# Kernel tuning notes

Measured on AMD Instinct MI355X. Metric: run time of the kernel, lower is better.

Reference implementation:

```python
import jax, jax.numpy as jnp
import numpy as np

B, H, W, C = 64, 28, 28, 384
G = 7
N = G * G                  # tokens per window = 49
NH, HD = 12, 32            # heads, head_dim
SCALE = HD ** -0.5
EPS = 1e-5


def _make_bias_coords():
    # biases: all relative (dh, dw) offsets, shape [(2G-1)^2, 2]
    r = np.arange(1 - G, G)
    biases = np.stack(np.meshgrid(r, r, indexing='ij')).reshape(2, -1).T.astype(np.float32)
    # relative_position_index: [N, N] lookup into the bias table
    coords = np.stack(np.meshgrid(np.arange(G), np.arange(G), indexing='ij')).reshape(2, -1)
    rel = coords[:, :, None] - coords[:, None, :]          # [2, N, N]
    rel = rel.transpose(1, 2, 0)                            # [N, N, 2]
    rel[:, :, 0] += G - 1
    rel[:, :, 1] += G - 1
    rel[:, :, 0] *= 2 * G - 1
    idx = rel.sum(-1)                                       # [N, N]
    return jnp.asarray(biases), jnp.asarray(idx, dtype=jnp.int32)

BIASES, REL_IDX = _make_bias_coords()


def _ln(x, g, b):
    m = jnp.mean(x, -1, keepdims=True)
    v = jnp.var(x, -1, keepdims=True)
    return (x - m) * jax.lax.rsqrt(v + EPS) * g + b


def _pos_bias(ppw, ppb, l1g, l1b, p1w, p1b, l2g, l2b, p2w, p2b, l3g, l3b, p3w, p3b):
    # DynamicPosBias with residual=False: pos3(pos2(pos1(pos_proj(biases))))
    pos = BIASES @ ppw + ppb                                # [169, 24]
    pos = jax.nn.relu(_ln(pos, l1g, l1b)) @ p1w + p1b
    pos = jax.nn.relu(_ln(pos, l2g, l2b)) @ p2w + p2b
    pos = jax.nn.relu(_ln(pos, l3g, l3b)) @ p3w + p3b       # [169, NH]
    # gather -> [N, N, NH] -> [NH, N, N]
    return pos[REL_IDX.reshape(-1)].reshape(N, N, NH).transpose(2, 0, 1)


def _forward(x, norm1_g, norm1_b, qkv_w, qkv_b, proj_w, proj_b,
             norm2_g, norm2_b, fc1_w, fc1_b, fc2_w, fc2_b,
             pp_w, pp_b, l1_g, l1_b, p1_w, p1_b, l2_g, l2_b, p2_w, p2_b,
             l3_g, l3_b, p3_w, p3_b):
    shortcut = x
    h = _ln(x, norm1_g, norm1_b).reshape(B, H, W, C)
    # SDA (lsda_flag=0) window partition: [B, H/G, G, W/G, G, C] -> windows
    h = h.reshape(B, H // G, G, W // G, G, C).transpose(0, 1, 3, 2, 4, 5)
    h = h.reshape(-1, N, C)                                 # [B*nW, N, C]
    Bw = h.shape[0]

    qkv = (h @ qkv_w + qkv_b).reshape(Bw, N, 3, NH, HD).transpose(2, 0, 3, 1, 4)
    q, k, v = qkv[0] * SCALE, qkv[1], qkv[2]                # [Bw, NH, N, HD]

    bias = _pos_bias(pp_w, pp_b, l1_g, l1_b, p1_w, p1_b,
                     l2_g, l2_b, p2_w, p2_b, l3_g, l3_b, p3_w, p3_b)
    attn = jnp.einsum('bhnd,bhmd->bhnm', q, k) + bias[None]  # [Bw, NH, N, N]
    attn = jax.nn.softmax(attn, axis=-1)

    o = jnp.einsum('bhnm,bhmd->bhnd', attn, v)
    o = o.transpose(0, 2, 1, 3).reshape(Bw, N, C)
    o = o @ proj_w + proj_b

    # reverse window partition
    o = o.reshape(B, H // G, W // G, G, G, C).transpose(0, 1, 3, 2, 4, 5)
    o = o.reshape(B, H * W, C)

    x = shortcut + o
    y = _ln(x, norm2_g, norm2_b)
    y = jax.nn.gelu(y @ fc1_w + fc1_b, approximate=False) @ fc2_w + fc2_b
    return x + y


def setup_inputs() -> dict:
    key = jax.random.key(0)
    ks = iter(jax.random.split(key, 32))
    s = 0.02
    PD = 24  # pos_dim = (dim // 4) // 4
    MH = 4 * C

    def rn(k, shape):
        return jax.random.normal(k, shape, dtype=jnp.float32) * s

    return {
        'x': jax.random.normal(next(ks), (B, H * W, C), dtype=jnp.float32),
        'norm1_g': jnp.ones((C,), jnp.float32), 'norm1_b': jnp.zeros((C,), jnp.float32),
        'qkv_w': rn(next(ks), (C, 3 * C)), 'qkv_b': jnp.zeros((3 * C,), jnp.float32),
        'proj_w': rn(next(ks), (C, C)), 'proj_b': jnp.zeros((C,), jnp.float32),
        'norm2_g': jnp.ones((C,), jnp.float32), 'norm2_b': jnp.zeros((C,), jnp.float32),
        'fc1_w': rn(next(ks), (C, MH)), 'fc1_b': jnp.zeros((MH,), jnp.float32),
        'fc2_w': rn(next(ks), (MH, C)), 'fc2_b': jnp.zeros((C,), jnp.float32),
        'pp_w': rn(next(ks), (2, PD)), 'pp_b': jnp.zeros((PD,), jnp.float32),
        'l1_g': jnp.ones((PD,), jnp.float32), 'l1_b': jnp.zeros((PD,), jnp.float32),
        'p1_w': rn(next(ks), (PD, PD)), 'p1_b': jnp.zeros((PD,), jnp.float32),
        'l2_g': jnp.ones((PD,), jnp.float32), 'l2_b': jnp.zeros((PD,), jnp.float32),
        'p2_w': rn(next(ks), (PD, PD)), 'p2_b': jnp.zeros((PD,), jnp.float32),
        'l3_g': jnp.ones((PD,), jnp.float32), 'l3_b': jnp.zeros((PD,), jnp.float32),
        'p3_w': rn(next(ks), (PD, NH)), 'p3_b': jnp.zeros((NH,), jnp.float32),
    }


def reference(x, norm1_g, norm1_b, qkv_w, qkv_b, proj_w, proj_b,
              norm2_g, norm2_b, fc1_w, fc1_b, fc2_w, fc2_b,
              pp_w, pp_b, l1_g, l1_b, p1_w, p1_b, l2_g, l2_b, p2_w, p2_b,
              l3_g, l3_b, p3_w, p3_b):
    return _forward(x, norm1_g, norm1_b, qkv_w, qkv_b, proj_w, proj_b,
                    norm2_g, norm2_b, fc1_w, fc1_b, fc2_w, fc2_b,
                    pp_w, pp_b, l1_g, l1_b, p1_w, p1_b, l2_g, l2_b, p2_w, p2_b,
                    l3_g, l3_b, p3_w, p3_b)
```

## Files before the change

kernel.cpp:

```cpp
#include <hip/hip_runtime.h>

typedef unsigned short u16;
typedef short s16x8 __attribute__((ext_vector_type(8)));
typedef short s16x4 __attribute__((ext_vector_type(4)));
typedef float f32x4 __attribute__((ext_vector_type(4)));
typedef float f32x2 __attribute__((ext_vector_type(2)));

#define B_ 64
#define Hh 28
#define Ww 28
#define Cc 384
#define Gg 7
#define Nn 49
#define NH 12
#define HD 32
#define TT 50176
#define NWIN 1024
#define QKV_ELEMS 19267584u
#define SCALE_Q 0.17677669529663687f

__device__ __forceinline__ float b2f(u16 u) {
  union { unsigned int i; float f; } v; v.i = ((unsigned int)u) << 16; return v.f;
}
__device__ __forceinline__ u16 f2b(float f) {
  union { float f; unsigned int i; } v; v.f = f;
  unsigned int r = v.i + 0x7fffu + ((v.i >> 16) & 1u);
  return (u16)(r >> 16);
}

__global__ void transpose_f2b(const float* __restrict__ in, u16* __restrict__ out,
                              int K, int N) {
  int i = blockIdx.x * 256 + threadIdx.x;
  if (i < K * N) {
    int k = i / N, n = i % N;
    out[(size_t)n * K + k] = f2b(in[i]);
  }
}

__global__ __launch_bounds__(256)
void pos_mlp_kernel(const float* __restrict__ pp_w, const float* __restrict__ pp_b,
                    const float* __restrict__ l1g, const float* __restrict__ l1b,
                    const float* __restrict__ p1w, const float* __restrict__ p1b,
                    const float* __restrict__ l2g, const float* __restrict__ l2b,
                    const float* __restrict__ p2w, const float* __restrict__ p2b,
                    const float* __restrict__ l3g, const float* __restrict__ l3b,
                    const float* __restrict__ p3w, const float* __restrict__ p3b,
                    float* __restrict__ pos169) {
  __shared__ float w0[48], bb0[24], g1[24], e1[24], w1[576], bb1[24],
                   g2[24], e2[24], w2[576], bb2[24], g3[24], e3[24], w3[288], bb3[12];
  int tid = threadIdx.x;
  for (int i = tid; i < 48; i += 256) w0[i] = pp_w[i];
  for (int i = tid; i < 24; i += 256) {
    bb0[i] = pp_b[i]; g1[i] = l1g[i]; e1[i] = l1b[i]; bb1[i] = p1b[i];
    g2[i] = l2g[i]; e2[i] = l2b[i]; bb2[i] = p2b[i];
    g3[i] = l3g[i]; e3[i] = l3b[i];
  }
  for (int i = tid; i < 576; i += 256) { w1[i] = p1w[i]; w2[i] = p2w[i]; }
  for (int i = tid; i < 288; i += 256) w3[i] = p3w[i];
  for (int i = tid; i < 12; i += 256) bb3[i] = p3b[i];
  __syncthreads();
  if (tid < 169) {
    float bi = (float)(tid / 13) - 6.f, bj = (float)(tid % 13) - 6.f;
    float cur[24], t[24];
    #pragma unroll
    for (int c = 0; c < 24; c++) cur[c] = bi * w0[c] + bj * w0[24 + c] + bb0[c];

    auto lnrelu = [&](const float* gg, const float* ee) {
      float s = 0.f, sq = 0.f;
      #pragma unroll
      for (int c = 0; c < 24; c++) { s += cur[c]; sq += cur[c] * cur[c]; }
      float mean = s * (1.f / 24.f);
      float var = sq * (1.f / 24.f) - mean * mean;
      float rstd = rsqrtf(var + 1e-5f);
      #pragma unroll
      for (int c = 0; c < 24; c++)
        t[c] = fmaxf(0.f, (cur[c] - mean) * rstd * gg[c] + ee[c]);
    };

    lnrelu(g1, e1);
    #pragma unroll
    for (int o = 0; o < 24; o++) {
      float a = bb1[o];
      #pragma unroll
      for (int c = 0; c < 24; c++) a += t[c] * w1[c * 24 + o];
      cur[o] = a;
    }
    lnrelu(g2, e2);
    #pragma unroll
    for (int o = 0; o < 24; o++) {
      float a = bb2[o];
      #pragma unroll
      for (int c = 0; c < 24; c++) a += t[c] * w2[c * 24 + o];
      cur[o] = a;
    }
    lnrelu(g3, e3);
    #pragma unroll
    for (int h = 0; h < 12; h++) {
      float a = bb3[h];
      #pragma unroll
      for (int c = 0; c < 24; c++) a += t[c] * w3[c * 12 + h];
      pos169[tid * 12 + h] = a;
    }
  }
}

__global__ __launch_bounds__(256)
void ln_kernel(const float* __restrict__ x, const float* __restrict__ g,
               const float* __restrict__ be, u16* __restrict__ out) {
  int wid = threadIdx.x >> 6, lane = threadIdx.x & 63;
  size_t row = (size_t)blockIdx.x * 4 + wid;
  const float* xr = x + row * Cc;
  float v[6];
  float s = 0.f, sq = 0.f;
  #pragma unroll
  for (int p = 0; p < 3; p++) {
    f32x2 u = *(const f32x2*)&xr[p * 128 + lane * 2];
    v[2 * p] = u.x; v[2 * p + 1] = u.y;
    s += u.x + u.y; sq += u.x * u.x + u.y * u.y;
  }
  #pragma unroll
  for (int off = 32; off > 0; off >>= 1) { s += __shfl_xor(s, off); sq += __shfl_xor(sq, off); }
  float mean = s * (1.f / 384.f);
  float var = sq * (1.f / 384.f) - mean * mean;
  float rstd = rsqrtf(var + 1e-5f);
  u16* orow = out + row * Cc;
  #pragma unroll
  for (int p = 0; p < 3; p++) {
    int c = p * 128 + lane * 2;
    f32x2 ug = *(const f32x2*)&g[c];
    f32x2 ub = *(const f32x2*)&be[c];
    float o0 = (v[2 * p] - mean) * rstd * ug.x + ub.x;
    float o1 = (v[2 * p + 1] - mean) * rstd * ug.y + ub.y;
    unsigned int uo = (unsigned int)f2b(o0) | ((unsigned int)f2b(o1) << 16);
    *(unsigned int*)&orow[c] = uo;
  }
}

template <int EPI>
__global__ __launch_bounds__(256, 2)
void gemm_k(const u16* __restrict__ A, const u16* __restrict__ Bt,
            const float* __restrict__ bias, const void* resv, void* outv,
            int M, int N, int K, int rowoff) {
  __shared__ u16 As[128 * 40];
  __shared__ u16 Bs[128 * 40];
  const int tid = threadIdx.x;
  const int mBase = blockIdx.y * 128;
  const int nBase = blockIdx.x * 128;
  const int wid = tid >> 6, lane = tid & 63;
  const int wr = (wid >> 1) * 64, wc = (wid & 1) * 64;
  const int lm = lane & 15, lq = lane >> 4;

  f32x4 acc[4][4] = {};
  for (int k0 = 0; k0 < K; k0 += 32) {
    #pragma unroll
    for (int ss = 0; ss < 2; ss++) {
      int li = tid + ss * 256;
      int r = li >> 2, c8 = (li & 3) * 8;
      *(s16x8*)&As[r * 40 + c8] = *(const s16x8*)&A[(size_t)(mBase + r) * K + k0 + c8];
      *(s16x8*)&Bs[r * 40 + c8] = *(const s16x8*)&Bt[(size_t)(nBase + r) * K + k0 + c8];
    }
    __syncthreads();
    s16x8 af[4], bfr[4];
    #pragma unroll
    for (int i = 0; i < 4; i++) af[i] = *(const s16x8*)&As[(wr + i * 16 + lm) * 40 + lq * 8];
    #pragma unroll
    for (int j = 0; j < 4; j++) bfr[j] = *(const s16x8*)&Bs[(wc + j * 16 + lm) * 40 + lq * 8];
    #pragma unroll
    for (int i = 0; i < 4; i++)
      #pragma unroll
      for (int j = 0; j < 4; j++)
        acc[i][j] = __builtin_amdgcn_mfma_f32_16x16x32_bf16(af[i], bfr[j], acc[i][j], 0, 0, 0);
    __syncthreads();
  }

  int colA[4]; float bvv[4];
  #pragma unroll
  for (int j = 0; j < 4; j++) {
    colA[j] = nBase + wc + j * 16 + lm;
    bvv[j] = bias[colA[j]];
  }

  if constexpr (EPI == 0) {
    u16* out = (u16*)outv;
    size_t offj[4]; float scl[4];
    #pragma unroll
    for (int j = 0; j < 4; j++) {
      int col = colA[j];
      int qi = col / 384, c2 = col % 384;
      int head = c2 >> 5, d = c2 & 31;
      offj[j] = (size_t)qi * QKV_ELEMS + (size_t)head * 1568 + d;
      scl[j] = (qi == 0) ? SCALE_Q : 1.0f;
    }
    #pragma unroll
    for (int i = 0; i < 4; i++) {
      #pragma unroll
      for (int rg = 0; rg < 4; rg++) {
        int t = mBase + wr + i * 16 + lq * 4 + rg;
        int b_ = t / 784, rr = t % 784;
        int hh = rr / 28, ww = rr % 28;
        int widx = b_ * 16 + (hh / 7) * 4 + (ww / 7);
        int n = (hh % 7) * 7 + (ww % 7);
        size_t offr = (size_t)widx * 18816 + n * 32;
        #pragma unroll
        for (int j = 0; j < 4; j++)
          out[offj[j] + offr] = f2b((acc[i][j][rg] + bvv[j]) * scl[j]);
      }
    }
  } else if constexpr (EPI == 1) {
    float* out = (float*)outv;
    const float* res = (const float*)resv;
    #pragma unroll
    for (int i = 0; i < 4; i++) {
      #pragma unroll
      for (int rg = 0; rg < 4; rg++) {
        size_t rb = (size_t)(rowoff + mBase + wr + i * 16 + lq * 4 + rg) * 384;
        #pragma unroll
        for (int j = 0; j < 4; j++) {
          size_t o = rb + colA[j];
          out[o] = acc[i][j][rg] + bvv[j] + res[o];
        }
      }
    }
  } else {
    u16* out = (u16*)outv;
    #pragma unroll
    for (int i = 0; i < 4; i++) {
      #pragma unroll
      for (int rg = 0; rg < 4; rg++) {
        size_t rb = (size_t)(mBase + wr + i * 16 + lq * 4 + rg) * 1536;
        #pragma unroll
        for (int j = 0; j < 4; j++) {
          float v = acc[i][j][rg] + bvv[j];
          float gl = 0.5f * v * (1.0f + erff(v * 0.70710678118654752f));
          out[rb + colA[j]] = f2b(gl);
        }
      }
    }
  }
}

__global__ __launch_bounds__(256, 3)
void attn_mfma(const u16* __restrict__ qkv, const float* __restrict__ pos169,
               u16* __restrict__ attn_out) {
  __shared__ u16 P_l[4][64 * 68];
  __shared__ float bias_l[4][170];
  const int wid = threadIdx.x >> 6, lane = threadIdx.x & 63;
  const int lm = lane & 15, lq = lane >> 4;
  const int pair = blockIdx.x * 4 + wid;
  const int widx = pair / 12, head = pair % 12;
  const u16* qp = qkv + (size_t)widx * 18816 + head * 1568;
  const u16* kp = qp + QKV_ELEMS;
  const u16* vp = kp + QKV_ELEMS;

  for (int i = lane; i < 169; i += 64) bias_l[wid][i] = pos169[i * 12 + head];

  s16x8 aq[4], bk[4];
  #pragma unroll
  for (int i = 0; i < 4; i++) aq[i] = *(const s16x8*)&qp[(i * 16 + lm) * 32 + lq * 8];
  #pragma unroll
  for (int j = 0; j < 4; j++) bk[j] = *(const s16x8*)&kp[(j * 16 + lm) * 32 + lq * 8];

  f32x4 acc[4][4] = {};
  #pragma unroll
  for (int i = 0; i < 4; i++)
    #pragma unroll
    for (int j = 0; j < 4; j++)
      acc[i][j] = __builtin_amdgcn_mfma_f32_16x16x32_bf16(aq[i], bk[j], acc[i][j], 0, 0, 0);

  int mj[4], mhj[4], mwj[4];
  #pragma unroll
  for (int j = 0; j < 4; j++) {
    mj[j] = j * 16 + lm; mhj[j] = mj[j] / 7; mwj[j] = mj[j] - mhj[j] * 7;
  }

  #pragma unroll
  for (int i = 0; i < 4; i++) {
    #pragma unroll
    for (int rg = 0; rg < 4; rg++) {
      int n = i * 16 + lq * 4 + rg;
      int nh = n / 7, nw = n - nh * 7;
      float s[4];
      #pragma unroll
      for (int j = 0; j < 4; j++) {
        int idx = (nh - mhj[j] + 6) * 13 + (nw - mwj[j] + 6);
        idx = min(max(idx, 0), 168);
        s[j] = acc[i][j][rg] + bias_l[wid][idx];
        if (mj[j] >= 49) s[j] = -3.0e30f;
      }
      float mx = fmaxf(fmaxf(s[0], s[1]), fmaxf(s[2], s[3]));
      #pragma unroll
      for (int off = 1; off < 16; off <<= 1) mx = fmaxf(mx, __shfl_xor(mx, off));
      float e[4];
      float sm = 0.f;
      #pragma unroll
      for (int j = 0; j < 4; j++) { e[j] = __expf(s[j] - mx); sm += e[j]; }
      #pragma unroll
      for (int off = 1; off < 16; off <<= 1) sm += __shfl_xor(sm, off);
      float r = 1.0f / sm;
      #pragma unroll
      for (int j = 0; j < 4; j++)
        P_l[wid][n * 68 + mj[j]] = f2b(e[j] * r);
    }
  }

  s16x8 ap[4][2];
  #pragma unroll
  for (int i = 0; i < 4; i++)
    #pragma unroll
    for (int ks = 0; ks < 2; ks++) {
      const u16* p = &P_l[wid][(i * 16 + lm) * 68 + ks * 32 + lq * 8];
      s16x4 lo = *(const s16x4*)p;
      s16x4 hi = *(const s16x4*)(p + 4);
      ap[i][ks] = __builtin_shufflevector(lo, hi, 0, 1, 2, 3, 4, 5, 6, 7);
    }
  s16x8 bv[2][2];
  #pragma unroll
  for (int jt = 0; jt < 2; jt++)
    #pragma unroll
    for (int ks = 0; ks < 2; ks++) {
      s16x8 v;
      #pragma unroll
      for (int jj = 0; jj < 8; jj++)
        v[jj] = (short)vp[(ks * 32 + lq * 8 + jj) * 32 + jt * 16 + lm];
      bv[jt][ks] = v;
    }

  f32x4 o[4][2] = {};
  #pragma unroll
  for (int i = 0; i < 4; i++)
    #pragma unroll
    for (int jt = 0; jt < 2; jt++)
      #pragma unroll
      for (int ks = 0; ks < 2; ks++)
        o[i][jt] = __builtin_amdgcn_mfma_f32_16x16x32_bf16(ap[i][ks], bv[jt][ks], o[i][jt], 0, 0, 0);

  const int b_ = widx >> 4, wq = widx & 15;
  const int hbase = (wq >> 2) * 7, wbase = (wq & 3) * 7;
  #pragma unroll
  for (int i = 0; i < 4; i++) {
    #pragma unroll
    for (int rg = 0; rg < 4; rg++) {
      int n = i * 16 + lq * 4 + rg;
      if (n < 49) {
        int nh = n / 7, nw = n - nh * 7;
        int t = b_ * 784 + (hbase + nh) * 28 + (wbase + nw);
        size_t ob = (size_t)t * 384 + head * 32 + lm;
        attn_out[ob] = f2b(o[i][0][rg]);
        attn_out[ob + 16] = f2b(o[i][1][rg]);
      }
    }
  }
}

extern "C" void kernel_launch(void* const* d_in, const int* in_sizes, int n_in,
                              void* d_out, int out_size, void* d_ws, size_t ws_size,
                              hipStream_t stream) {
  const float* x      = (const float*)d_in[0];
  const float* n1g    = (const float*)d_in[1];
  const float* n1b    = (const float*)d_in[2];
  const float* qkv_w  = (const float*)d_in[3];
  const float* qkv_b  = (const float*)d_in[4];
  const float* proj_w = (const float*)d_in[5];
  const float* proj_b = (const float*)d_in[6];
  const float* n2g    = (const float*)d_in[7];
  const float* n2b    = (const float*)d_in[8];
  const float* fc1_w  = (const float*)d_in[9];
  const float* fc1_b  = (const float*)d_in[10];
  const float* fc2_w  = (const float*)d_in[11];
  const float* fc2_b  = (const float*)d_in[12];

  const size_t SZ_A = 115605504;
  const size_t SZ_B = 38535168;
  char* wsb = (char*)d_ws;
  u16* regA     = (u16*)wsb;
  u16* regB     = (u16*)(wsb + SZ_A);
  float* pos169 = (float*)(wsb + SZ_A + SZ_B);
  u16* qkvT     = (u16*)(wsb + SZ_A + SZ_B + 8192);
  u16* projT    = qkvT + 442368;
  u16* fc1T     = projT + 147456;
  u16* fc2T     = fc1T + 589824;

  float* out = (float*)d_out;

  transpose_f2b<<<1728, 256, 0, stream>>>(qkv_w, qkvT, 384, 1152);
  transpose_f2b<<<576, 256, 0, stream>>>(proj_w, projT, 384, 384);
  transpose_f2b<<<2304, 256, 0, stream>>>(fc1_w, fc1T, 384, 1536);
  transpose_f2b<<<2304, 256, 0, stream>>>(fc2_w, fc2T, 1536, 384);

  pos_mlp_kernel<<<1, 256, 0, stream>>>(
      (const float*)d_in[13], (const float*)d_in[14], (const float*)d_in[15], (const float*)d_in[16],
      (const float*)d_in[17], (const float*)d_in[18], (const float*)d_in[19], (const float*)d_in[20],
      (const float*)d_in[21], (const float*)d_in[22], (const float*)d_in[23], (const float*)d_in[24],
      (const float*)d_in[25], (const float*)d_in[26], pos169);

  ln_kernel<<<TT / 4, 256, 0, stream>>>(x, n1g, n1b, regB);

  gemm_k<0><<<dim3(9, 392), 256, 0, stream>>>(regB, qkvT, qkv_b, nullptr, regA,
                                              TT, 1152, 384, 0);

  attn_mfma<<<NWIN * NH / 4, 256, 0, stream>>>(regA, pos169, regB);

  gemm_k<1><<<dim3(3, 392), 256, 0, stream>>>(regB, projT, proj_b, x, out,
                                              TT, 384, 384, 0);

  ln_kernel<<<TT / 4, 256, 0, stream>>>(out, n2g, n2b, regB);

  for (int ch = 0; ch < 2; ch++) {
    const u16* h2c = regB + (size_t)ch * 25088 * 384;
    gemm_k<2><<<dim3(12, 196), 256, 0, stream>>>(h2c, fc1T, fc1_b, nullptr, regA,
                                                 25088, 1536, 384, 0);
    gemm_k<1><<<dim3(3, 196), 256, 0, stream>>>(regA, fc2T, fc2_b, out, out,
                                                25088, 384, 1536, ch * 25088);
  }
}
```

Measured before the change: 765.5 us.

## Use direct global-to-LDS loads with XOR swizzle and XCD-aware tile mapping in GEMM

The GEMM tile loads now go straight from global memory into LDS through global_load_lds, so the data no longer passes through registers. The LDS tiles use an unpadded, XOR-swizzled layout to avoid bank conflicts, which also lets the launch bound ask for 4 blocks per CU. Block indices are remapped to a 1D grid so that consecutive tiles land on the same XCD, which should improve L2 locality. The swizzle has to match on both the write and read sides, and the larger occupancy target may cap registers for the 4x4 accumulator tile.

```diff
diff --git a/kernel.cpp b/kernel.cpp
--- a/kernel.cpp
+++ b/kernel.cpp
@@ -26,6 +26,12 @@
   union { float f; unsigned int i; } v; v.f = f;
   unsigned int r = v.i + 0x7fffu + ((v.i >> 16) & 1u);
   return (u16)(r >> 16);
+}
+
+__device__ __forceinline__ void gload_lds16(const u16* g, u16* l) {
+  __builtin_amdgcn_global_load_lds(
+      (const __attribute__((address_space(1))) unsigned int*)(const void*)g,
+      (__attribute__((address_space(3))) unsigned int*)(void*)l, 16, 0, 0);
 }
 
 __global__ void transpose_f2b(const float* __restrict__ in, u16* __restrict__ out,
@@ -137,34 +143,60 @@
 }
 
 template <int EPI>
-__global__ __launch_bounds__(256, 2)
+__global__ __launch_bounds__(256, 4)
 void gemm_k(const u16* __restrict__ A, const u16* __restrict__ Bt,
             const float* __restrict__ bias, const void* resv, void* outv,
-            int M, int N, int K, int rowoff) {
-  __shared__ u16 As[128 * 40];
-  __shared__ u16 Bs[128 * 40];
+            int K, int gridX, int rowoff) {
+  __shared__ u16 As[128 * 32];
+  __shared__ u16 Bs[128 * 32];
   const int tid = threadIdx.x;
-  const int mBase = blockIdx.y * 128;
-  const int nBase = blockIdx.x * 128;
   const int wid = tid >> 6, lane = tid & 63;
   const int wr = (wid >> 1) * 64, wc = (wid & 1) * 64;
   const int lm = lane & 15, lq = lane >> 4;
 
+  {
+  }
+  const int total = gridDim.x;
+  const int xcd = blockIdx.x & 7, pos = blockIdx.x >> 3;
+  const int cbase = total >> 3, crem = total & 7;
+  const int tile = (xcd < crem) ? (xcd * (cbase + 1) + pos)
+                                : (crem * (cbase + 1) + (xcd - crem) * cbase + pos);
+  const int mTile = tile / gridX;
+  const int nTile = tile - mTile * gridX;
+  const int mBase = mTile * 128, nBase = nTile * 128;
+
+  const int srow = tid >> 2;
+  const int sg = (tid & 3) ^ ((tid >> 3) & 3);
+  const size_t aRow0 = (size_t)(mBase + srow) * K + sg * 8;
+  const size_t aRow1 = (size_t)(mBase + 64 + srow) * K + sg * 8;
+  const size_t bRow0 = (size_t)(nBase + srow) * K + sg * 8;
+  const size_t bRow1 = (size_t)(nBase + 64 + srow) * K + sg * 8;
+  u16* aDst0 = As + tid * 8;
+  u16* aDst1 = As + 2048 + tid * 8;
+  u16* bDst0 = Bs + tid * 8;
+  u16* bDst1 = Bs + 2048 + tid * 8;
+
+  int aslot[4], bslot[4];
+  #pragma unroll
+  for (int i = 0; i < 4; i++) {
+    int ar = wr + i * 16 + lm;
+    aslot[i] = ar * 32 + (lq ^ ((ar >> 1) & 3)) * 8;
+    int br = wc + i * 16 + lm;
+    bslot[i] = br * 32 + (lq ^ ((br >> 1) & 3)) * 8;
+  }
+
   f32x4 acc[4][4] = {};
   for (int k0 = 0; k0 < K; k0 += 32) {
-    #pragma unroll
-    for (int ss = 0; ss < 2; ss++) {
-      int li = tid + ss * 256;
-      int r = li >> 2, c8 = (li & 3) * 8;
-      *(s16x8*)&As[r * 40 + c8] = *(const s16x8*)&A[(size_t)(mBase + r) * K + k0 + c8];
-      *(s16x8*)&Bs[r * 40 + c8] = *(const s16x8*)&Bt[(size_t)(nBase + r) * K + k0 + c8];
-    }
+    gload_lds16(A + aRow0 + k0, aDst0);
+    gload_lds16(A + aRow1 + k0, aDst1);
+    gload_lds16(Bt + bRow0 + k0, bDst0);
+    gload_lds16(Bt + bRow1 + k0, bDst1);
     __syncthreads();
     s16x8 af[4], bfr[4];
     #pragma unroll
-    for (int i = 0; i < 4; i++) af[i] = *(const s16x8*)&As[(wr + i * 16 + lm) * 40 + lq * 8];
-    #pragma unroll
-    for (int j = 0; j < 4; j++) bfr[j] = *(const s16x8*)&Bs[(wc + j * 16 + lm) * 40 + lq * 8];
+    for (int i = 0; i < 4; i++) af[i] = *(const s16x8*)&As[aslot[i]];
+    #pragma unroll
+    for (int j = 0; j < 4; j++) bfr[j] = *(const s16x8*)&Bs[bslot[j]];
     #pragma unroll
     for (int i = 0; i < 4; i++)
       #pragma unroll
@@ -395,21 +427,21 @@
 
   ln_kernel<<<TT / 4, 256, 0, stream>>>(x, n1g, n1b, regB);
 
-  gemm_k<0><<<dim3(9, 392), 256, 0, stream>>>(regB, qkvT, qkv_b, nullptr, regA,
-                                              TT, 1152, 384, 0);
+  gemm_k<0><<<392 * 9, 256, 0, stream>>>(regB, qkvT, qkv_b, nullptr, regA,
+                                         384, 9, 0);
 
   attn_mfma<<<NWIN * NH / 4, 256, 0, stream>>>(regA, pos169, regB);
 
-  gemm_k<1><<<dim3(3, 392), 256, 0, stream>>>(regB, projT, proj_b, x, out,
-                                              TT, 384, 384, 0);
+  gemm_k<1><<<392 * 3, 256, 0, stream>>>(regB, projT, proj_b, x, out,
+                                         384, 3, 0);
 
   ln_kernel<<<TT / 4, 256, 0, stream>>>(out, n2g, n2b, regB);
 
   for (int ch = 0; ch < 2; ch++) {
     const u16* h2c = regB + (size_t)ch * 25088 * 384;
-    gemm_k<2><<<dim3(12, 196), 256, 0, stream>>>(h2c, fc1T, fc1_b, nullptr, regA,
-                                                 25088, 1536, 384, 0);
-    gemm_k<1><<<dim3(3, 196), 256, 0, stream>>>(regA, fc2T, fc2_b, out, out,
-                                                25088, 384, 1536, ch * 25088);
-  }
-}
+    gemm_k<2><<<196 * 12, 256, 0, stream>>>(h2c, fc1T, fc1_b, nullptr, regA,
+                                            384, 12, 0);
+    gemm_k<1><<<196 * 3, 256, 0, stream>>>(regA, fc2T, fc2_b, out, out,
+                                           1536, 3, ch * 25088);
+  }
+}
```

After: 664.2 us. 1.15x faster.
